# Kernel tuning notes

Measured on AMD Instinct MI355X. Metric: run time of the kernel, lower is better.

The kernel has to match this reference:

```python
import jax, jax.numpy as jnp
import numpy as np

TEMP = 0.5
K_SEL = 20
NEG_SLOPE = 0.1


def setup_inputs() -> dict:
    key = jax.random.key(0)
    ks = jax.random.split(key, 12)
    B, N = 64, 20000
    F1, F2, D = 512, 256, 128
    init = lambda k, shape, fan: (jax.random.normal(k, shape) / np.sqrt(fan)).astype(jnp.float32)
    return {
        "patient_embedding": jax.random.normal(ks[0], (B, F1), dtype=jnp.float32),
        "gene_embedding": jax.random.normal(ks[1], (N, F2), dtype=jnp.float32),
        "Wq": init(ks[2], (F1, D), F1), "bq": jnp.zeros((D,), jnp.float32),
        "Wk": init(ks[3], (F2, D), F2), "bk": jnp.zeros((D,), jnp.float32),
        "Wv": init(ks[4], (F2, D), F2), "bv": jnp.zeros((D,), jnp.float32),
        "W1": init(ks[5], (2 * D, D), 2 * D), "b1": jnp.zeros((D,), jnp.float32),
        "w2": init(ks[6], (D,), D), "b2": jnp.zeros((), jnp.float32),
    }


def reference(patient_embedding, gene_embedding, Wq, bq, Wk, bk, Wv, bv, W1, b1, w2, b2):
    B = patient_embedding.shape[0]
    N = gene_embedding.shape[0]
    D = Wq.shape[1]

    Q = patient_embedding @ Wq + bq          # [B, D]
    Km = gene_embedding @ Wk + bk            # [N, D]
    V = gene_embedding @ Wv + bv             # [N, D]

    # MLP attention on cat([Q_exp, K_exp]); split W1 to avoid materializing [B,N,2D]
    q_part = Q @ W1[:D]                      # [B, D]
    k_part = Km @ W1[D:]                     # [N, D]
    h = jax.nn.leaky_relu(q_part[:, None, :] + k_part[None, :, :] + b1, NEG_SLOPE)  # [B, N, D]
    sim = h @ w2 + b2                        # [B, N]
    logits = sim / TEMP

    # gumbel-softmax, hard=True, independent noise per (b, k) row
    g = jax.random.gumbel(jax.random.key(42), (B, K_SEL, N), dtype=logits.dtype)
    y_soft = jax.nn.softmax((logits[:, None, :] + g) / TEMP, axis=-1)   # [B, K, N]
    y_hard = jax.nn.one_hot(jnp.argmax(y_soft, axis=-1), N, dtype=y_soft.dtype)
    masks = y_hard - jax.lax.stop_gradient(y_soft) + y_soft             # straight-through

    topk_values = jnp.einsum("bkn,nd->bkd", masks, V)                   # [B, K, D]
    scores = jnp.einsum("bd,bkd->bk", Q, topk_values) / np.sqrt(D).astype(np.float32)
    weights = jax.nn.softmax(scores, axis=-1)                           # [B, K] (dropout = eval/identity)
    context = jnp.einsum("bk,bkd->bd", weights, topk_values)            # [B, D]
    return context
```

## Files before the change

kernel.cpp:

```cpp
#include <hip/hip_runtime.h>

#define NG 20000

__device__ __forceinline__ unsigned rotl32(unsigned x, int r) {
  return __builtin_amdgcn_alignbit(x, x, 32 - r);
}

__device__ __forceinline__ void threefry2x32(unsigned x0, unsigned x1,
                                             unsigned& o0, unsigned& o1) {
  const unsigned ks0 = 0u;
  const unsigned ks1 = 42u;
  const unsigned ks2 = 0x1BD11BDAu ^ 0u ^ 42u;
  x0 += ks0; x1 += ks1;
#define TFR(r) { x0 += x1; x1 = rotl32(x1, (r)); x1 ^= x0; }
  TFR(13) TFR(15) TFR(26) TFR(6)
  x0 += ks1; x1 += ks2 + 1u;
  TFR(17) TFR(29) TFR(16) TFR(24)
  x0 += ks2; x1 += ks0 + 2u;
  TFR(13) TFR(15) TFR(26) TFR(6)
  x0 += ks0; x1 += ks1 + 3u;
  TFR(17) TFR(29) TFR(16) TFR(24)
  x0 += ks1; x1 += ks2 + 4u;
  TFR(13) TFR(15) TFR(26) TFR(6)
  x0 += ks2; x1 += ks0 + 5u;
#undef TFR
  o0 = x0; o1 = x1;
}

__device__ __forceinline__ unsigned tfbits(unsigned ctr) {
  unsigned o0, o1;
  threefry2x32(0u, ctr, o0, o1);
  return o0 ^ o1;
}

__device__ __forceinline__ float gumbel32(unsigned bits) {
  float f = __uint_as_float((bits >> 9) | 0x3f800000u) - 1.0f;
  float u = fmaxf(f, 1.17549435e-38f);
  const float l2u = __log2f(u);
  return fmaf(-0.69314718056f, __log2f(-l2u), 0.3665129206f);
}

__device__ __forceinline__ double gumbel64(unsigned bits) {
  float f = __uint_as_float((bits >> 9) | 0x3f800000u) - 1.0f;
  double u = (double)fmaxf(f, 1.17549435e-38f);
  return -log(-log(u));
}

__device__ __forceinline__ unsigned long long packcell(double v, int n) {
  unsigned long long u = (unsigned long long)__double_as_longlong(v);
  u = (u >> 63) ? ~u : (u | 0x8000000000000000ull);
  return (u & 0xFFFFFFFFFFFF8000ull) | (unsigned long long)(32767 - n);
}

__device__ __forceinline__ unsigned long long packscreen(float v, int n) {
  unsigned u = __float_as_uint(v);
  u = (u >> 31) ? ~u : (u | 0x80000000u);
  return ((unsigned long long)u << 32) | (unsigned)n;
}

__global__ __launch_bounds__(128) void kprep(
    const float* __restrict__ pe, const float* __restrict__ Wq,
    const float* __restrict__ bq, const float* __restrict__ Wk,
    const float* __restrict__ bk, const float* __restrict__ W1,
    const float* __restrict__ b1, const float* __restrict__ w2,
    float* __restrict__ Wf32, double* __restrict__ qbT,
    float* __restrict__ Qm, unsigned long long* __restrict__ cells,
    double2* __restrict__ c12) {
  __shared__ float L[512];
  __shared__ double Ld[128];
  const int t = threadIdx.x;
  const int bid = blockIdx.x;
  if (bid < 256) {
    L[t] = Wk[bid * 128 + t];
    __syncthreads();
    double acc = 0.0;
    #pragma unroll 16
    for (int j = 0; j < 128; ++j)
      acc = fma((double)L[j], (double)W1[(128 + j) * 128 + t], acc);
    Wf32[bid * 128 + t] = (float)acc;
  } else if (bid < 320) {
    const int b = bid - 256;
    #pragma unroll
    for (int i = 0; i < 4; ++i) L[t + 128 * i] = pe[b * 512 + t + 128 * i];
    __syncthreads();
    double q = (double)bq[t];
    #pragma unroll 16
    for (int f = 0; f < 512; ++f)
      q = fma((double)L[f], (double)Wq[f * 128 + t], q);
    Qm[b * 128 + t] = (float)q;
    Ld[t] = q;
    __syncthreads();
    double acc = (double)b1[t];
    #pragma unroll 8
    for (int j = 0; j < 128; ++j) {
      acc = fma(Ld[j], (double)W1[j * 128 + t], acc);
      acc = fma((double)bk[j], (double)W1[(128 + j) * 128 + t], acc);
    }
    qbT[t * 64 + b] = acc;
  } else {
    for (int i = t; i < 1280; i += 128) cells[i] = 0ull;
    const double w2d = (double)w2[t];
    c12[t] = make_double2(0.55 * w2d, 0.45 * w2d);
  }
}

__global__ __launch_bounds__(256) void ksim(
    const float* __restrict__ ge, const float* __restrict__ Wf32,
    const double* __restrict__ qbT, const double2* __restrict__ c12,
    float* __restrict__ simg) {
  __shared__ double SBd[2048];
  __shared__ float Wt[4096];
  __shared__ float kpL[2048];
  float* geL = (float*)SBd;
  float* simLf = (float*)SBd;
  const int t = threadIdx.x;
  const int wv = t >> 6;
  const int lane = t & 63;
  const int g0 = blockIdx.x * 16;

  {
    const float4* src = (const float4*)(ge + (size_t)g0 * 256);
    float4* dst = (float4*)geL;
    #pragma unroll
    for (int i = 0; i < 4; ++i) dst[t + i * 256] = src[t + i * 256];
  }

  float acc[4][2];
  #pragma unroll
  for (int j = 0; j < 4; ++j) { acc[j][0] = 0.f; acc[j][1] = 0.f; }
  const float* gL = geL + wv * 4 * 256;

  for (int tile = 0; tile < 8; ++tile) {
    __syncthreads();
    {
      const float4* wsrc = (const float4*)(Wf32 + tile * 32 * 128);
      float4* wdst = (float4*)Wt;
      #pragma unroll
      for (int i = 0; i < 4; ++i) wdst[t + i * 256] = wsrc[t + i * 256];
    }
    __syncthreads();
    #pragma unroll
    for (int fr = 0; fr < 32; fr += 4) {
      const int f0 = tile * 32 + fr;
      const float2 w0 = *(const float2*)(Wt + (fr + 0) * 128 + 2 * lane);
      const float2 w1 = *(const float2*)(Wt + (fr + 1) * 128 + 2 * lane);
      const float2 w2 = *(const float2*)(Wt + (fr + 2) * 128 + 2 * lane);
      const float2 w3 = *(const float2*)(Wt + (fr + 3) * 128 + 2 * lane);
      #pragma unroll
      for (int j = 0; j < 4; ++j) {
        const float4 gv = *(const float4*)(gL + j * 256 + f0);
        acc[j][0] = fmaf(gv.x, w0.x, acc[j][0]);
        acc[j][1] = fmaf(gv.x, w0.y, acc[j][1]);
        acc[j][0] = fmaf(gv.y, w1.x, acc[j][0]);
        acc[j][1] = fmaf(gv.y, w1.y, acc[j][1]);
        acc[j][0] = fmaf(gv.z, w2.x, acc[j][0]);
        acc[j][1] = fmaf(gv.z, w2.y, acc[j][1]);
        acc[j][0] = fmaf(gv.w, w3.x, acc[j][0]);
        acc[j][1] = fmaf(gv.w, w3.y, acc[j][1]);
      }
    }
  }

  __syncthreads();
  #pragma unroll
  for (int j = 0; j < 4; ++j)
    ((float2*)(kpL + (wv * 4 + j) * 128))[lane] =
        make_float2(acc[j][0], acc[j][1]);
  __syncthreads();

  double s[4];
  #pragma unroll
  for (int j = 0; j < 4; ++j) s[j] = 0.0;
  for (int dd = 0; dd < 128; ++dd) {
    const double2 cc = c12[dd];
    const double qv = qbT[dd * 64 + lane];
    #pragma unroll
    for (int j = 0; j < 4; ++j) {
      const double kv = (double)kpL[(wv + j * 4) * 128 + dd];
      const double tt = qv + kv;
      s[j] = fma(tt, cc.x, s[j]);
      s[j] = fma(fabs(tt), cc.y, s[j]);
    }
  }
  #pragma unroll
  for (int j = 0; j < 4; ++j)
    simLf[lane * 17 + (wv + j * 4)] = (float)(2.0 * s[j]);
  __syncthreads();

  {
    const int b = t >> 2;
    const int gc = t & 3;
    float4 v;
    v.x = simLf[b * 17 + gc * 4 + 0];
    v.y = simLf[b * 17 + gc * 4 + 1];
    v.z = simLf[b * 17 + gc * 4 + 2];
    v.w = simLf[b * 17 + gc * 4 + 3];
    *(float4*)(simg + (size_t)b * NG + g0 + gc * 4) = v;
  }
}

__global__ __launch_bounds__(256) void kargmax(
    const float* __restrict__ simg, unsigned long long* __restrict__ cells) {
  __shared__ unsigned long long R1s[4], R2s[4];
  const int cell = blockIdx.x >> 1;
  const int wdw = blockIdx.x & 1;
  const int t = threadIdx.x;
  const int wv = t >> 6;
  const int lane = t & 63;
  const int b = (unsigned)cell / 20u;
  const float* sb = simg + (size_t)b * NG;
  const unsigned ib = (unsigned)cell * (unsigned)NG;
  const int base = wdw * 10000;

  float m1 = -3e38f, m2 = -3e38f;
  int n1 = -1, n2 = -1;
  for (int c = t; c < 2500; c += 256) {
    const int n0 = base + c * 4;
    const float4 sv = *(const float4*)(sb + n0);
    const unsigned bb0 = tfbits(ib + (unsigned)n0);
    const unsigned bb1 = tfbits(ib + (unsigned)(n0 + 1));
    const unsigned bb2 = tfbits(ib + (unsigned)(n0 + 2));
    const unsigned bb3 = tfbits(ib + (unsigned)(n0 + 3));
    const float s0 = sv.x + gumbel32(bb0);
    const float s1 = sv.y + gumbel32(bb1);
    const float s2 = sv.z + gumbel32(bb2);
    const float s3 = sv.w + gumbel32(bb3);
    if (s0 > m1) { m2 = m1; n2 = n1; m1 = s0; n1 = n0; }
    else if (s0 > m2) { m2 = s0; n2 = n0; }
    if (s1 > m1) { m2 = m1; n2 = n1; m1 = s1; n1 = n0 + 1; }
    else if (s1 > m2) { m2 = s1; n2 = n0 + 1; }
    if (s2 > m1) { m2 = m1; n2 = n1; m1 = s2; n1 = n0 + 2; }
    else if (s2 > m2) { m2 = s2; n2 = n0 + 2; }
    if (s3 > m1) { m2 = m1; n2 = n1; m1 = s3; n1 = n0 + 3; }
    else if (s3 > m2) { m2 = s3; n2 = n0 + 3; }
  }
  unsigned long long p1 = packscreen(m1, n1);
  unsigned long long p2 = packscreen(m2, n2);
  #pragma unroll
  for (int off = 32; off; off >>= 1) {
    unsigned long long q1 = __shfl_xor(p1, off, 64);
    unsigned long long q2 = __shfl_xor(p2, off, 64);
    if (q1 > p1) {
      unsigned long long t1 = p1;
      p1 = q1;
      p2 = (q2 > t1) ? q2 : t1;
    } else {
      p2 = (q1 > p2) ? q1 : p2;
    }
  }
  if (lane == 0) { R1s[wv] = p1; R2s[wv] = p2; }
  __syncthreads();
  if (t == 0) {
    unsigned long long P1 = R1s[0], P2 = R2s[0];
    #pragma unroll
    for (int w = 1; w < 4; ++w) {
      unsigned long long q1 = R1s[w], q2 = R2s[w];
      if (q1 > P1) {
        unsigned long long t1 = P1;
        P1 = q1;
        P2 = (q2 > t1) ? q2 : t1;
      } else {
        P2 = (q1 > P2) ? q1 : P2;
      }
    }
    const int w1 = (int)(P1 & 0xFFFFFFFFull);
    const int w2i = (int)(P2 & 0xFFFFFFFFull);
    const unsigned bb1 = tfbits(ib + (unsigned)w1);
    const float s1f = sb[w1];
    const float sc1 = s1f + gumbel32(bb1);
    unsigned long long pb = packcell((double)s1f + gumbel64(bb1), w1);
    if (w2i >= 0) {
      const unsigned bb2 = tfbits(ib + (unsigned)w2i);
      const float s2f = sb[w2i];
      const float sc2 = s2f + gumbel32(bb2);
      if ((sc1 - sc2) < 1e-4f) {
        const unsigned long long u2 =
            packcell((double)s2f + gumbel64(bb2), w2i);
        if (u2 > pb) pb = u2;
      }
    }
    atomicMax(&cells[cell], pb);
  }
}

__global__ __launch_bounds__(256) void kfinal(
    const float* __restrict__ ge, const float* __restrict__ Wv,
    const float* __restrict__ bv, const float* __restrict__ Qm,
    const unsigned long long* __restrict__ cells, float* __restrict__ out) {
  const int b = blockIdx.x;
  const int t = threadIdx.x;
  const int wv = t >> 6;
  const int lane = t & 63;
  __shared__ float sc[20];
  __shared__ float ctxp[4][128];
  const float2 qv = ((const float2*)(Qm + b * 128))[lane];
  const float2 bvv = ((const float2*)bv)[lane];
  const float* gr[5];
  float2 V[5];
  #pragma unroll
  for (int j = 0; j < 5; ++j) {
    const unsigned long long cell = cells[b * 20 + wv * 5 + j];
    const int n = 32767 - (int)(cell & 0x7FFFull);
    gr[j] = ge + (size_t)n * 256;
    V[j] = bvv;
  }
  for (int f = 0; f < 256; f += 4) {
    const float2 w0 = ((const float2*)(Wv + (size_t)(f + 0) * 128))[lane];
    const float2 w1 = ((const float2*)(Wv + (size_t)(f + 1) * 128))[lane];
    const float2 w2_ = ((const float2*)(Wv + (size_t)(f + 2) * 128))[lane];
    const float2 w3 = ((const float2*)(Wv + (size_t)(f + 3) * 128))[lane];
    #pragma unroll
    for (int j = 0; j < 5; ++j) {
      const float4 gv = *(const float4*)(gr[j] + f);
      V[j].x = fmaf(gv.x, w0.x, V[j].x); V[j].y = fmaf(gv.x, w0.y, V[j].y);
      V[j].x = fmaf(gv.y, w1.x, V[j].x); V[j].y = fmaf(gv.y, w1.y, V[j].y);
      V[j].x = fmaf(gv.z, w2_.x, V[j].x); V[j].y = fmaf(gv.z, w2_.y, V[j].y);
      V[j].x = fmaf(gv.w, w3.x, V[j].x); V[j].y = fmaf(gv.w, w3.y, V[j].y);
    }
  }
  #pragma unroll
  for (int j = 0; j < 5; ++j) {
    float pr = qv.x * V[j].x + qv.y * V[j].y;
    #pragma unroll
    for (int off = 32; off; off >>= 1) pr += __shfl_xor(pr, off, 64);
    if (lane == 0) sc[wv * 5 + j] = pr * 0.08838834764831845f;
  }
  __syncthreads();
  float m = -3.0e38f;
  #pragma unroll
  for (int i = 0; i < 20; ++i) m = fmaxf(m, sc[i]);
  float s = 0.f;
  #pragma unroll
  for (int i = 0; i < 20; ++i) s += expf(sc[i] - m);
  const float inv = 1.0f / s;
  float c0 = 0.f, c1 = 0.f;
  #pragma unroll
  for (int j = 0; j < 5; ++j) {
    const float wk = expf(sc[wv * 5 + j] - m) * inv;
    c0 = fmaf(wk, V[j].x, c0);
    c1 = fmaf(wk, V[j].y, c1);
  }
  ctxp[wv][2 * lane] = c0;
  ctxp[wv][2 * lane + 1] = c1;
  __syncthreads();
  if (t < 128)
    out[b * 128 + t] = (ctxp[0][t] + ctxp[1][t]) + (ctxp[2][t] + ctxp[3][t]);
}

extern "C" void kernel_launch(void* const* d_in, const int* in_sizes, int n_in,
                              void* d_out, int out_size, void* d_ws, size_t ws_size,
                              hipStream_t stream) {
  (void)in_sizes; (void)n_in; (void)out_size; (void)ws_size;
  const float* pe = (const float*)d_in[0];
  const float* ge = (const float*)d_in[1];
  const float* Wq = (const float*)d_in[2];
  const float* bq = (const float*)d_in[3];
  const float* Wk = (const float*)d_in[4];
  const float* bk = (const float*)d_in[5];
  const float* Wv = (const float*)d_in[6];
  const float* bvp = (const float*)d_in[7];
  const float* W1 = (const float*)d_in[8];
  const float* b1 = (const float*)d_in[9];
  const float* w2 = (const float*)d_in[10];

  char* w = (char*)d_ws;
  float* Wf32 = (float*)w;
  double* qbT = (double*)(w + 131072);
  float* Qm = (float*)(w + 196608);
  unsigned long long* cells =
      (unsigned long long*)(w + 229376);
  double2* c12 = (double2*)(w + 239616);
  float* simg = (float*)(w + 262144);
  float* out = (float*)d_out;

  kprep<<<dim3(321), dim3(128), 0, stream>>>(pe, Wq, bq, Wk, bk, W1, b1, w2,
                                             Wf32, qbT, Qm, cells, c12);
  ksim<<<dim3(1250), dim3(256), 0, stream>>>(ge, Wf32, qbT, c12, simg);
  kargmax<<<dim3(2560), dim3(256), 0, stream>>>(simg, cells);
  kfinal<<<dim3(64), dim3(256), 0, stream>>>(ge, Wv, bvp, Qm, cells, out);
}
```

Baseline: 261.7 us.

## Register-prefetch next W tile during compute in K-projection kernel

The weight tile load is software-pipelined through registers. The next tile's global load is issued before computing on the current LDS tile, and full __syncthreads are replaced with lgkmcnt waits plus raw s_barrier. The aim is to hide global-memory latency behind the FMA loop. In exchange it uses more registers, and correctness now depends on the compiler inserting vmcnt waits before the register values are stored to LDS.

```diff
diff --git a/kernel.cpp b/kernel.cpp
--- a/kernel.cpp
+++ b/kernel.cpp
@@ -129,16 +129,9 @@
   #pragma unroll
   for (int j = 0; j < 4; ++j) { acc[j][0] = 0.f; acc[j][1] = 0.f; }
   const float* gL = geL + wv * 4 * 256;
-
-  for (int tile = 0; tile < 8; ++tile) {
-    __syncthreads();
-    {
-      const float4* wsrc = (const float4*)(Wf32 + tile * 32 * 128);
-      float4* wdst = (float4*)Wt;
-      #pragma unroll
-      for (int i = 0; i < 4; ++i) wdst[t + i * 256] = wsrc[t + i * 256];
-    }
-    __syncthreads();
+  const float4* wsrc = (const float4*)Wf32;
+
+  auto compute = [&](int tile) {
     #pragma unroll
     for (int fr = 0; fr < 32; fr += 4) {
       const int f0 = tile * 32 + fr;
@@ -159,6 +152,43 @@
         acc[j][1] = fmaf(gv.w, w3.y, acc[j][1]);
       }
     }
+  };
+
+  float4 wrA[4], wrB[4];
+  #pragma unroll
+  for (int i = 0; i < 4; ++i) wrA[i] = wsrc[t + i * 256];
+
+  for (int tp = 0; tp < 4; ++tp) {
+    asm volatile("s_waitcnt lgkmcnt(0)" ::: "memory");
+    __builtin_amdgcn_s_barrier();
+    {
+      float4* wdst = (float4*)Wt;
+      #pragma unroll
+      for (int i = 0; i < 4; ++i) wdst[t + i * 256] = wrA[i];
+    }
+    {
+      const float4* s2 = wsrc + (2 * tp + 1) * 1024;
+      #pragma unroll
+      for (int i = 0; i < 4; ++i) wrB[i] = s2[t + i * 256];
+    }
+    asm volatile("s_waitcnt lgkmcnt(0)" ::: "memory");
+    __builtin_amdgcn_s_barrier();
+    compute(2 * tp);
+    asm volatile("s_waitcnt lgkmcnt(0)" ::: "memory");
+    __builtin_amdgcn_s_barrier();
+    {
+      float4* wdst = (float4*)Wt;
+      #pragma unroll
+      for (int i = 0; i < 4; ++i) wdst[t + i * 256] = wrB[i];
+    }
+    if (tp < 3) {
+      const float4* s2 = wsrc + (2 * tp + 2) * 1024;
+      #pragma unroll
+      for (int i = 0; i < 4; ++i) wrA[i] = s2[t + i * 256];
+    }
+    asm volatile("s_waitcnt lgkmcnt(0)" ::: "memory");
+    __builtin_amdgcn_s_barrier();
+    compute(2 * tp + 1);
   }
 
   __syncthreads();
```

Result: slower. 282.5 us (+7.9%).
